# Kernel tuning notes

Measured on AMD Instinct MI355X. Metric: run time of the kernel, lower is better.

Reference implementation:

```python
import jax, jax.numpy as jnp
import numpy as np


def _conv(x, w, b=None, stride=1, pad=1, groups=1):
    y = jax.lax.conv_general_dilated(
        x, w, (stride, stride), [(pad, pad), (pad, pad)],
        dimension_numbers=('NCHW', 'OIHW', 'NCHW'), feature_group_count=groups)
    return y if b is None else y + b[None, :, None, None]


def _dwt(x):
    # Haar DWT as grouped stride-2 conv, filters pre-flipped as in the torch code
    ll = np.array([[0.5, 0.5], [0.5, 0.5]])
    lh = np.array([[-0.5, -0.5], [0.5, 0.5]])
    hl = np.array([[-0.5, 0.5], [-0.5, 0.5]])
    hh = np.array([[0.5, -0.5], [-0.5, 0.5]])
    filts = np.stack([f[None, ::-1, ::-1] for f in (ll, lh, hl, hh)], 0)  # [4,1,2,2]
    w = jnp.asarray(np.concatenate([filts] * 3, 0), x.dtype)  # [12,1,2,2], groups=3
    return _conv(x, w, None, stride=2, pad=0, groups=3)


def setup_inputs():
    key = jax.random.key(0)
    ks = iter(jax.random.split(key, 64))
    def w(*shape):
        return jax.random.normal(next(ks), shape, jnp.float32) * 0.05
    B, H, W = 4, 512, 512
    F = 32  # number_f
    d = {'x': jax.random.uniform(next(ks), (B, 3, H, W), jnp.float32)}
    d['enc1_w'] = w(F, 3, 3, 3); d['enc1_b'] = w(F)
    for i in range(2, 6):
        d['enc%d_w' % i] = w(F, F, 3, 3); d['enc%d_b' % i] = w(F)
    d['cdc_w'] = w(F, F, 3, 3)                      # central-difference conv, no bias
    d['ct_w'] = w(64, 9, 3, 3); d['ct_b'] = w(64)   # conv_theta on 9-ch high_freq
    d['t1_w'] = w(64, 64, 1, 1); d['t1_b'] = w(64)
    d['t2_w'] = w(64, 64, 1, 1); d['t2_b'] = w(64)
    d['t3_w'] = w(1, 64, 1, 1); d['t3_b'] = w(1)
    d['lf_w'] = w(64, 3, 3, 3); d['lf_b'] = w(64)   # low_freq conv on haar_A
    d['fc1_w'] = w(512, 64); d['fc1_b'] = w(512)
    d['fc2_w'] = w(512, 512); d['fc2_b'] = w(512)
    d['fc3_w'] = w(512, 512); d['fc3_b'] = w(512)
    d['g_w'] = w(F, 512); d['g_b'] = w(F)           # to_gamma_0
    d['be_w'] = w(F, 512); d['be_b'] = w(F)         # to_beta_0
    d['res_w'] = w(F, F, 3, 3); d['res_b'] = w(F)
    d['d1_w'] = w(F, F, 3, 3); d['d1_b'] = w(F)
    d['d2_w'] = w(1, F, 3, 3); d['d2_b'] = w(1)
    return d


def reference(x, enc1_w, enc1_b, enc2_w, enc2_b, enc3_w, enc3_b, enc4_w, enc4_b,
              enc5_w, enc5_b, cdc_w, ct_w, ct_b, t1_w, t1_b, t2_w, t2_b, t3_w, t3_b,
              lf_w, lf_b, fc1_w, fc1_b, fc2_w, fc2_b, fc3_w, fc3_b,
              g_w, g_b, be_w, be_b, res_w, res_b, d1_w, d1_b, d2_w, d2_b):
    relu = jax.nn.relu
    # encoder
    f = relu(_conv(x, enc1_w, enc1_b))
    f = relu(_conv(f, enc2_w, enc2_b))
    f = relu(_conv(f, enc3_w, enc3_b))
    f = relu(_conv(f, enc4_w, enc4_b))
    f_org4 = relu(_conv(f, enc5_w, enc5_b))  # [B,32,H,W]
    # Haar wavelet split: per input channel blocks of 4 = (A,H,V,D)
    dwt = _dwt(x)                             # [B,12,H/2,W/2]
    haar_A = dwt[:, 0::4]                     # c1,c5,c9
    high_freq = jnp.concatenate([dwt[:, 1::4], dwt[:, 2::4], dwt[:, 3::4]], 1)  # [B,9,...]
    # theta net (Conv2d_cd)
    a = relu(_conv(high_freq, ct_w, ct_b))
    a = a.mean((2, 3), keepdims=True)         # adaptive avg pool to 1x1
    a = relu(_conv(a, t1_w, t1_b, pad=0))
    a = relu(_conv(a, t2_w, t2_b, pad=0))
    theta = jax.nn.sigmoid(_conv(a, t3_w, t3_b, pad=0))   # [B,1,1,1]
    out_normal = _conv(f_org4, cdc_w, None)
    kdiff = cdc_w.sum((2, 3))[:, :, None, None]            # [32,32,1,1]
    out_diff = _conv(f_org4, kdiff, None, pad=0)
    f_deco = relu(out_normal - theta * out_diff)           # [B,32,H,W]
    # attention / FiLM branch
    am = relu(_conv(haar_A, lf_w, lf_b)).mean((2, 3))      # [B,64]
    am = relu(am @ fc1_w.T + fc1_b)
    am = relu(am @ fc2_w.T + fc2_b)
    am = jax.nn.sigmoid(am @ fc3_w.T + fc3_b)              # [B,512]
    gamma = jax.nn.sigmoid(am @ g_w.T + g_b)[:, :, None, None]  # [B,32,1,1]
    beta = jnp.tanh(am @ be_w.T + be_b)[:, :, None, None]
    f = f_deco + gamma * _conv(f_deco, res_w, res_b) + beta
    # decoder
    f = relu(_conv(f, d1_w, d1_b))
    out_map = jnp.tanh(_conv(f, d2_w, d2_b))               # [B,1,H,W]
    enhance_image = x + out_map * (x * x - x)
    return enhance_image, out_map
```

## Files before the change

kernel.cpp:

```cpp
#include <hip/hip_runtime.h>
#include <hip/hip_bf16.h>
#include <cmath>

#define TPB 256

typedef __attribute__((ext_vector_type(8))) short s16x8;
typedef __attribute__((ext_vector_type(4))) float f32x4;
typedef unsigned short ushortT;

constexpr long long PSTR = 8454272;
constexpr int HW = 512 * 512;

static __device__ __forceinline__ short f2bf(float f) {
    union { __hip_bfloat16 h; short s; } u;
    u.h = __float2bfloat16(f);
    return u.s;
}
static __device__ __forceinline__ float bf2f(unsigned short u) {
    union { unsigned int i; float f; } v;
    v.i = ((unsigned int)u) << 16;
    return v.f;
}
static __device__ __forceinline__ unsigned int pack2(float a, float b) {
    return (unsigned int)(unsigned short)f2bf(a) | ((unsigned int)(unsigned short)f2bf(b) << 16);
}

#define GLOAD_LDS16(gp, lp) \
    __builtin_amdgcn_global_load_lds((const __attribute__((address_space(1))) void*)(gp), \
                                     (__attribute__((address_space(3))) void*)(lp), 16, 0, 0)

static __device__ void pack_body(const float* w, const float* bias, const float* theta,
                                 short* dst, int CO, int CI_src, int ci_off, int cog, int l)
{
    const int l15 = l & 15, sl = l >> 4;
    for (int t = 0; t < 9; ++t) {
        for (int mt = 0; mt < 2; ++mt) {
            const int co = cog * 32 + 16 * mt + l15;
            s16x8 p;
            #pragma unroll
            for (int i = 0; i < 8; ++i) {
                const int pci = 8 * sl + i;
                float val = 0.f;
                if (co < CO && pci >= ci_off && pci < ci_off + CI_src) {
                    const int ci = pci - ci_off;
                    val = w[((size_t)co * CI_src + ci) * 9 + t];
                    if (theta && t == 4) {
                        float s = 0.f;
                        for (int tt = 0; tt < 9; ++tt) s += w[((size_t)co * CI_src + ci) * 9 + tt];
                        val -= theta[0] * s;
                    }
                }
                p[i] = f2bf(val);
            }
            *(s16x8*)(dst + ((size_t)(t * 2 + mt) * 64 + l) * 8) = p;
        }
    }
    if (l < 32) {
        const int co = cog * 32 + l;
        ((float*)(dst + 9216))[l] = (bias && co < CO) ? bias[co] : 0.f;
    }
}

__global__ __launch_bounds__(64) void packall_k(
    const float* e1w, const float* e1b, const float* e2w, const float* e2b,
    const float* e3w, const float* e3b, const float* e4w, const float* e4b,
    const float* e5w, const float* e5b, const float* resw, const float* resb,
    const float* d1w, const float* d1b, const float* d2w, const float* d2b,
    const float* ctw, const float* ctb, const float* lfw, const float* lfb,
    short* wpack)
{
    const int s = blockIdx.x;
    const float *w, *b;
    int CO = 32, CI = 32, coff = 0, cog = 0;
    switch (s) {
        case 0: w = e1w; b = e1b; CI = 3; break;
        case 1: w = e2w; b = e2b; break;
        case 2: w = e3w; b = e3b; break;
        case 3: w = e4w; b = e4b; break;
        case 4: w = e5w; b = e5b; break;
        case 5: w = resw; b = resb; break;
        case 6: w = d1w; b = d1b; break;
        case 7: w = d2w; b = d2b; CO = 1; break;
        case 8: case 9: w = ctw; b = ctb; CO = 64; CI = 9; cog = s - 8; break;
        default: w = lfw; b = lfb; CO = 64; CI = 3; coff = 9; cog = s - 10; break;
    }
    pack_body(w, b, nullptr, wpack + (size_t)s * 10240, CO, CI, coff, cog, threadIdx.x);
}

__global__ __launch_bounds__(64) void packcdc_k(
    const float* cdcw, const float* theta, short* wpack)
{
    const int b = blockIdx.x;
    pack_body(cdcw, nullptr, theta + b, wpack + (size_t)(12 + b) * 10240, 32, 32, 0, 0, threadIdx.x);
}

__global__ __launch_bounds__(TPB) void zero_k(unsigned int* A2u, unsigned int* B2u)
{
    const int idx = blockIdx.x * TPB + threadIdx.x;
    if (idx >= 8 * 32832) return;
    const int q = idx / 32832, r = idx % 32832;
    unsigned int* P = (q < 4 ? A2u : B2u) + (size_t)(q & 3) * 4227136;
    const int RSU = 514 * 16;
    int off;
    if (r < 8224)       off = r;
    else if (r < 16448) off = 513 * RSU + (r - 8224);
    else if (r < 24640) { int u = r - 16448; off = (1 + (u >> 4)) * RSU + (u & 15); }
    else                { int u = r - 24640; off = (1 + (u >> 4)) * RSU + 513 * 16 + (u & 15); }
    P[off] = 0u;
}

__global__ __launch_bounds__(TPB) void ctlf_k(
    const float* __restrict__ x0p, const short* __restrict__ wpack8,
    float* __restrict__ part)
{
    constexpr int RSX = 66;
    constexpr int ROWB = RSX * 64;
    __shared__ s16x8 lds_t[6 * RSX * 4];
    __shared__ float s_red[4][32];
    char* sb = (char*)lds_t;

    const int z = blockIdx.z, cog = blockIdx.y;
    const int bid = blockIdx.x;
    const int x0 = (bid & 3) * 64, y0 = (bid >> 2) * 4;
    const int tid = threadIdx.x, lane = tid & 63, wv = tid >> 6;
    const int l15 = lane & 15, slot = lane >> 4;

    const short* wslot = wpack8 + (size_t)cog * 10240;
    const float* xz = x0p + (size_t)z * 3 * HW;

    s16x8 wf[9][2];
    #pragma unroll
    for (int t = 0; t < 9; ++t)
        #pragma unroll
        for (int mt = 0; mt < 2; ++mt)
            wf[t][mt] = *(const s16x8*)(wslot + ((size_t)(t * 2 + mt) * 64 + lane) * 8);

    #pragma unroll
    for (int j = 0; j < 2; ++j) {
        const int p = j * 256 + tid;
        if (p < 396) {
            const int row = p / 66, lx = p - row * 66;
            const int vs = (lx + (lx >> 2)) & 3;
            char* base = sb + (row * RSX + lx) * 64;
            const int sy = y0 + row - 1, sx = x0 + lx - 1;
            s16x8 pk0, pk1, zz;
            #pragma unroll
            for (int i = 0; i < 8; ++i) { pk0[i] = 0; pk1[i] = 0; zz[i] = 0; }
            if (sy >= 0 && sy < 256 && sx >= 0 && sx < 256) {
                #pragma unroll
                for (int c = 0; c < 3; ++c) {
                    const float* xp = xz + ((size_t)c * 512 + 2 * sy) * 512 + 2 * sx;
                    const float2 tp = *(const float2*)xp;
                    const float2 bt = *(const float2*)(xp + 512);
                    const float a = tp.x, b = tp.y, cc = bt.x, d = bt.y;
                    pk0[c]     = f2bf(0.5f * (a + b - cc - d));
                    pk0[3 + c] = f2bf(0.5f * (a - b + cc - d));
                    const float hh = 0.5f * (a - b - cc + d);
                    const float ll = 0.5f * (a + b + cc + d);
                    if (c < 2) pk0[6 + c] = f2bf(hh);
                    else       pk1[0]     = f2bf(hh);
                    pk1[1 + c] = f2bf(ll);
                }
            }
            *(s16x8*)(base + ((0 ^ vs) << 4)) = pk0;
            *(s16x8*)(base + ((1 ^ vs) << 4)) = pk1;
            *(s16x8*)(base + ((2 ^ vs) << 4)) = zz;
            *(s16x8*)(base + ((3 ^ vs) << 4)) = zz;
        }
    }
    __syncthreads();

    const int xw = 16 * wv;
    int roff[3];
    #pragma unroll
    for (int dx = 0; dx < 3; ++dx) {
        const int lx = xw + dx + l15;
        const int vs = (lx + (lx >> 2)) & 3;
        roff[dx] = lx * 64 + ((slot ^ vs) << 4);
    }
    const float* bptr = (const float*)(wslot + 9216);

    float ps[2][4];
    #pragma unroll
    for (int mt = 0; mt < 2; ++mt)
        #pragma unroll
        for (int reg = 0; reg < 4; ++reg) ps[mt][reg] = 0.f;

    #pragma unroll
    for (int r2 = 0; r2 < 4; r2 += 2) {
        f32x4 acc[2][2];
        #pragma unroll
        for (int a = 0; a < 2; ++a)
            #pragma unroll
            for (int b = 0; b < 2; ++b)
                #pragma unroll
                for (int e = 0; e < 4; ++e) acc[a][b][e] = 0.f;

        #pragma unroll
        for (int dy = 0; dy < 3; ++dy) {
            const int rb0 = (r2 + dy) * ROWB;
            #pragma unroll
            for (int dx = 0; dx < 3; ++dx) {
                const int tap = dy * 3 + dx;
                const s16x8 b0 = *(const s16x8*)(sb + rb0 + roff[dx]);
                const s16x8 b1 = *(const s16x8*)(sb + rb0 + ROWB + roff[dx]);
                #pragma unroll
                for (int mt = 0; mt < 2; ++mt) {
                    acc[0][mt] = __builtin_amdgcn_mfma_f32_16x16x32_bf16(wf[tap][mt], b0, acc[0][mt], 0, 0, 0);
                    acc[1][mt] = __builtin_amdgcn_mfma_f32_16x16x32_bf16(wf[tap][mt], b1, acc[1][mt], 0, 0, 0);
                }
            }
        }

        #pragma unroll
        for (int rr = 0; rr < 2; ++rr)
            #pragma unroll
            for (int mt = 0; mt < 2; ++mt)
                #pragma unroll
                for (int reg = 0; reg < 4; ++reg)
                    ps[mt][reg] += fmaxf(acc[rr][mt][reg] + bptr[16 * mt + 4 * slot + reg], 0.f);
    }

    #pragma unroll
    for (int mt = 0; mt < 2; ++mt)
        #pragma unroll
        for (int reg = 0; reg < 4; ++reg) {
            #pragma unroll
            for (int o = 1; o < 16; o <<= 1)
                ps[mt][reg] += __shfl_xor(ps[mt][reg], o, 64);
        }
    #pragma unroll
    for (int mt = 0; mt < 2; ++mt)
        #pragma unroll
        for (int reg = 0; reg < 4; ++reg)
            if (l15 == mt * 4 + reg)
                s_red[wv][16 * mt + 4 * slot + reg] = ps[mt][reg];
    __syncthreads();
    if (tid < 32) {
        const float s = s_red[0][tid] + s_red[1][tid] + s_red[2][tid] + s_red[3][tid];
        part[(((size_t)z * 4 + cog) * 256 + bid) * 32 + tid] = s;
    }
}

__global__ __launch_bounds__(TPB) void enc1n_k(
    const float* __restrict__ x0p, const short* __restrict__ wslot,
    ushortT* __restrict__ outP0)
{
    constexpr int RSX = 66;
    constexpr int ROWB = RSX * 64;
    __shared__ s16x8 lds_t[6 * RSX * 4];
    char* sb = (char*)lds_t;

    const int z = blockIdx.z;
    const float* xin = x0p + (size_t)z * 3 * HW;

    const int tid = threadIdx.x, lane = tid & 63, wv = tid >> 6;
    const int bid = blockIdx.x;
    const int swz = (bid & 7) * 128 + (bid >> 3);
    const int x0 = (swz & 7) * 64, y0 = (swz >> 3) * 4;
    const int l15 = lane & 15, slot = lane >> 4;

    s16x8 wf[9][2];
    #pragma unroll
    for (int t = 0; t < 9; ++t)
        #pragma unroll
        for (int mt = 0; mt < 2; ++mt)
            wf[t][mt] = *(const s16x8*)(wslot + ((size_t)(t * 2 + mt) * 64 + lane) * 8);

    #pragma unroll
    for (int j = 0; j < 2; ++j) {
        const int p = j * 256 + tid;
        if (p < 396) {
            const int row = p / 66, lx = p - row * 66;
            const int vs = (lx + (lx >> 2)) & 3;
            char* base = sb + (row * RSX + lx) * 64;
            const int gy = y0 + row - 1, gx = x0 + lx - 1;
            s16x8 pk, zz;
            #pragma unroll
            for (int i = 0; i < 8; ++i) { pk[i] = 0; zz[i] = 0; }
            if (gy >= 0 && gy < 512 && gx >= 0 && gx < 512) {
                #pragma unroll
                for (int c = 0; c < 3; ++c)
                    pk[c] = f2bf(xin[((size_t)c * 512 + gy) * 512 + gx]);
            }
            *(s16x8*)(base + ((0 ^ vs) << 4)) = pk;
            *(s16x8*)(base + ((1 ^ vs) << 4)) = zz;
            *(s16x8*)(base + ((2 ^ vs) << 4)) = zz;
            *(s16x8*)(base + ((3 ^ vs) << 4)) = zz;
        }
    }
    __syncthreads();

    const int xw = 16 * wv;
    int roff[3];
    #pragma unroll
    for (int dx = 0; dx < 3; ++dx) {
        const int lx = xw + dx + l15;
        const int vs = (lx + (lx >> 2)) & 3;
        roff[dx] = lx * 64 + ((slot ^ vs) << 4);
    }
    const float* bptr = (const float*)(wslot + 9216);
    ushortT* outP = outP0 + (size_t)z * PSTR;

    #pragma unroll
    for (int r2 = 0; r2 < 4; r2 += 2) {
        f32x4 acc[2][2];
        #pragma unroll
        for (int a = 0; a < 2; ++a)
            #pragma unroll
            for (int b = 0; b < 2; ++b)
                #pragma unroll
                for (int e = 0; e < 4; ++e) acc[a][b][e] = 0.f;

        #pragma unroll
        for (int dy = 0; dy < 3; ++dy) {
            const int rb0 = (r2 + dy) * ROWB;
            #pragma unroll
            for (int dx = 0; dx < 3; ++dx) {
                const int tap = dy * 3 + dx;
                const s16x8 b0 = *(const s16x8*)(sb + rb0 + roff[dx]);
                const s16x8 b1 = *(const s16x8*)(sb + rb0 + ROWB + roff[dx]);
                #pragma unroll
                for (int mt = 0; mt < 2; ++mt) {
                    acc[0][mt] = __builtin_amdgcn_mfma_f32_16x16x32_bf16(wf[tap][mt], b0, acc[0][mt], 0, 0, 0);
                    acc[1][mt] = __builtin_amdgcn_mfma_f32_16x16x32_bf16(wf[tap][mt], b1, acc[1][mt], 0, 0, 0);
                }
            }
        }

        #pragma unroll
        for (int rr = 0; rr < 2; ++rr) {
            const int gy = y0 + r2 + rr;
            const int gx = x0 + xw + l15;
            #pragma unroll
            for (int mt = 0; mt < 2; ++mt) {
                const size_t off = ((size_t)(gy + 1) * 514 + gx + 1) * 32 + 16 * mt + 4 * slot;
                float v[4];
                #pragma unroll
                for (int reg = 0; reg < 4; ++reg)
                    v[reg] = fmaxf(acc[rr][mt][reg] + bptr[16 * mt + 4 * slot + reg], 0.f);
                *(uint2*)(outP + off) = make_uint2(pack2(v[0], v[1]), pack2(v[2], v[3]));
            }
        }
    }
}

template<int EPI>
__global__ __launch_bounds__(TPB) void dconv64p_k(
    const ushortT* __restrict__ inP0, const short* __restrict__ wbase, int wstr,
    ushortT* __restrict__ outP0,
    const float* __restrict__ gamma0, const float* __restrict__ beta0,
    const float* __restrict__ xorig0, float* __restrict__ outE0, float* __restrict__ outM0)
{
    constexpr int MT = (EPI == 3) ? 1 : 2;
    constexpr int RSX = 66;
    constexpr int ROWB = RSX * 64;
    constexpr int BUFB = 6 * RSX * 64;
    __shared__ s16x8 lds_t[2 * 6 * RSX * 4];
    char* sbase = (char*)lds_t;

    const int z = blockIdx.z;
    const ushortT* inP = inP0 + (size_t)z * PSTR;
    const short* wslot = wbase + (size_t)z * wstr;

    const int tid = threadIdx.x, lane = tid & 63, wv = tid >> 6;
    const int bid = blockIdx.x;
    const int xcd = bid & 7, idx = bid >> 3;
    const int x0 = (idx & 7) * 64;
    const int yband = xcd * 4 + (idx >> 3);
    const int l15 = lane & 15, slot = lane >> 4;

    s16x8 wf[9][MT];
    #pragma unroll
    for (int t = 0; t < 9; ++t)
        #pragma unroll
        for (int mt = 0; mt < MT; ++mt)
            wf[t][mt] = *(const s16x8*)(wslot + ((size_t)(t * 2 + mt) * 64 + lane) * 8);

    const int xw = 16 * wv;
    int roff[3];
    #pragma unroll
    for (int dx = 0; dx < 3; ++dx) {
        const int lx = xw + dx + l15;
        const int vs = (lx + (lx >> 2)) & 3;
        roff[dx] = lx * 64 + ((slot ^ vs) << 4);
    }
    const float* bptr = (const float*)(wslot + 9216);

    auto stage = [&](int t, int b) {
        const int y0 = yband * 16 + 4 * t;
        char* sb = sbase + b * BUFB;
        #pragma unroll
        for (int j = 0; j < 6; ++j) {
            const int p = j * 256 + tid;
            const int row = p / 264;
            const int rem = p - row * 264;
            const int lx = rem >> 2, osl = rem & 3;
            const int o = osl ^ ((lx + (lx >> 2)) & 3);
            const ushortT* gp = inP + ((size_t)(y0 + row) * 514 + x0 + lx) * 32 + o * 8;
            GLOAD_LDS16(gp, sb + (size_t)(j * 256 + wv * 64) * 16);
        }
        if (tid < 48) {
            const int p = 1536 + tid;
            const int row = p / 264;
            const int rem = p - row * 264;
            const int lx = rem >> 2, osl = rem & 3;
            const int o = osl ^ ((lx + (lx >> 2)) & 3);
            const ushortT* gp = inP + ((size_t)(y0 + row) * 514 + x0 + lx) * 32 + o * 8;
            GLOAD_LDS16(gp, sb + (size_t)1536 * 16);
        }
    };

    stage(0, 0);

    #pragma unroll 1
    for (int t = 0; t < 4; ++t) {
        __syncthreads();
        if (t < 3) stage(t + 1, (t + 1) & 1);
        char* sb = sbase + (t & 1) * BUFB;
        const int y0t = yband * 16 + 4 * t;

        #pragma unroll
        for (int r2 = 0; r2 < 4; r2 += 2) {
            f32x4 acc[2][MT];
            #pragma unroll
            for (int a = 0; a < 2; ++a)
                #pragma unroll
                for (int b = 0; b < MT; ++b)
                    #pragma unroll
                    for (int e = 0; e < 4; ++e) acc[a][b][e] = 0.f;

            #pragma unroll
            for (int dy = 0; dy < 3; ++dy) {
                const int rb0 = (r2 + dy) * ROWB;
                #pragma unroll
                for (int dx = 0; dx < 3; ++dx) {
                    const int tap = dy * 3 + dx;
                    const s16x8 b0 = *(const s16x8*)(sb + rb0 + roff[dx]);
                    const s16x8 b1 = *(const s16x8*)(sb + rb0 + ROWB + roff[dx]);
                    #pragma unroll
                    for (int mt = 0; mt < MT; ++mt) {
                        acc[0][mt] = __builtin_amdgcn_mfma_f32_16x16x32_bf16(wf[tap][mt], b0, acc[0][mt], 0, 0, 0);
                        acc[1][mt] = __builtin_amdgcn_mfma_f32_16x16x32_bf16(wf[tap][mt], b1, acc[1][mt], 0, 0, 0);
                    }
                }
            }

            #pragma unroll
            for (int rr = 0; rr < 2; ++rr) {
                const int gy = y0t + r2 + rr;
                const int gx = x0 + xw + l15;
                if constexpr (EPI == 3) {
                    if (slot == 0) {
                        const float* xorig = xorig0 + (size_t)z * 3 * HW;
                        float* outE = outE0 + (size_t)z * 3 * HW;
                        float* outM = outM0 + (size_t)z * HW;
                        const float om = tanhf(acc[rr][0][0] + bptr[0]);
                        outM[(size_t)gy * 512 + gx] = om;
                        #pragma unroll
                        for (int c = 0; c < 3; ++c) {
                            const size_t xi = ((size_t)c * 512 + gy) * 512 + gx;
                            const float xv = xorig[xi];
                            outE[xi] = xv + om * (xv * xv - xv);
                        }
                    }
                } else {
                    ushortT* outP = outP0 + (size_t)z * PSTR;
                    #pragma unroll
                    for (int mt = 0; mt < MT; ++mt) {
                        const size_t off = ((size_t)(gy + 1) * 514 + gx + 1) * 32 + 16 * mt + 4 * slot;
                        float v[4];
                        #pragma unroll
                        for (int reg = 0; reg < 4; ++reg)
                            v[reg] = acc[rr][mt][reg] + bptr[16 * mt + 4 * slot + reg];
                        if constexpr (EPI == 0) {
                            #pragma unroll
                            for (int reg = 0; reg < 4; ++reg) v[reg] = fmaxf(v[reg], 0.f);
                        } else if constexpr (EPI == 2) {
                            const int prow = r2 + rr + 1;
                            const int lxr = xw + l15 + 1;
                            const int vsr = (lxr + (lxr >> 2)) & 3;
                            const int oo = (2 * mt + (slot >> 1)) ^ vsr;
                            const uint2 din = *(const uint2*)(sb + (prow * RSX + lxr) * 64 + (oo << 4) + ((slot & 1) << 3));
                            const float* gamma = gamma0 + 32 * z;
                            const float* beta  = beta0 + 32 * z;
                            const int cb = 16 * mt + 4 * slot;
                            v[0] = bf2f((unsigned short)(din.x & 0xffff)) + gamma[cb + 0] * v[0] + beta[cb + 0];
                            v[1] = bf2f((unsigned short)(din.x >> 16))    + gamma[cb + 1] * v[1] + beta[cb + 1];
                            v[2] = bf2f((unsigned short)(din.y & 0xffff)) + gamma[cb + 2] * v[2] + beta[cb + 2];
                            v[3] = bf2f((unsigned short)(din.y >> 16))    + gamma[cb + 3] * v[3] + beta[cb + 3];
                        }
                        *(uint2*)(outP + off) = make_uint2(pack2(v[0], v[1]), pack2(v[2], v[3]));
                    }
                }
            }
        }
    }
}

__global__ __launch_bounds__(TPB) void meanfin_k(
    const float* __restrict__ part, float* __restrict__ amean, float* __restrict__ am0)
{
    const int br = blockIdx.x;
    const int o = threadIdx.x;
    const int z = o >> 6, co = o & 63;
    const int cog = (br ? 2 : 0) + (co >> 5), c = co & 31;
    const float* p = part + (((size_t)z * 4 + cog) * 256) * 32 + c;
    float s = 0.f;
    for (int j = 0; j < 256; ++j) s += p[j * 32];
    (br ? am0 : amean)[z * 64 + co] = s * (1.f / 65536.f);
}

__global__ __launch_bounds__(64) void tchain_k(
    const float* __restrict__ amean,
    const float* __restrict__ t1w, const float* __restrict__ t1b,
    const float* __restrict__ t2w, const float* __restrict__ t2b,
    const float* __restrict__ t3w, const float* __restrict__ t3b,
    float* __restrict__ theta)
{
    const int b = blockIdx.x;
    const float* am = amean + b * 64;
    __shared__ float a0[64], a1[64], a2[64];
    const int co = threadIdx.x;
    a0[co] = am[co];
    __syncthreads();
    float s = t1b[co];
    #pragma unroll 8
    for (int ci = 0; ci < 64; ++ci) s = fmaf(t1w[co * 64 + ci], a0[ci], s);
    a1[co] = fmaxf(s, 0.f);
    __syncthreads();
    s = t2b[co];
    #pragma unroll 8
    for (int ci = 0; ci < 64; ++ci) s = fmaf(t2w[co * 64 + ci], a1[ci], s);
    a2[co] = fmaxf(s, 0.f);
    __syncthreads();
    if (co == 0) {
        float v = t3b[0];
        for (int ci = 0; ci < 64; ++ci) v = fmaf(t3w[ci], a2[ci], v);
        theta[b] = 1.f / (1.f + expf(-v));
    }
}

template<int ACT>
__global__ __launch_bounds__(TPB) void fcw_k(
    const float* __restrict__ in, const float* __restrict__ w,
    const float* __restrict__ bias, float* __restrict__ out, int K, int N)
{
    const int lane = threadIdx.x & 63, wv = threadIdx.x >> 6;
    const int idx = blockIdx.x * 4 + wv;
    if (idx >= 4 * N) return;
    const int b = idx / N, co = idx % N;
    float s = 0.f;
    for (int k = lane * 4; k < K; k += 256) {
        const float4 wv4 = *(const float4*)(w + (size_t)co * K + k);
        const float4 iv  = *(const float4*)(in + (size_t)b * K + k);
        s += wv4.x * iv.x + wv4.y * iv.y + wv4.z * iv.z + wv4.w * iv.w;
    }
    #pragma unroll
    for (int o = 32; o > 0; o >>= 1) s += __shfl_xor(s, o, 64);
    if (lane == 0) {
        s += bias[co];
        if (ACT == 0) s = fmaxf(s, 0.f);
        else if (ACT == 1) s = 1.f / (1.f + expf(-s));
        else s = tanhf(s);
        out[(size_t)b * N + co] = s;
    }
}

extern "C" void kernel_launch(void* const* d_in, const int* in_sizes, int n_in,
                              void* d_out, int out_size, void* d_ws, size_t ws_size,
                              hipStream_t stream)
{
    const float* x      = (const float*)d_in[0];
    const float* cdc_w  = (const float*)d_in[11];
    const float* t1_w   = (const float*)d_in[14];
    const float* t1_b   = (const float*)d_in[15];
    const float* t2_w   = (const float*)d_in[16];
    const float* t2_b   = (const float*)d_in[17];
    const float* t3_w   = (const float*)d_in[18];
    const float* t3_b   = (const float*)d_in[19];
    const float* fc1_w  = (const float*)d_in[22];
    const float* fc1_b  = (const float*)d_in[23];
    const float* fc2_w  = (const float*)d_in[24];
    const float* fc2_b  = (const float*)d_in[25];
    const float* fc3_w  = (const float*)d_in[26];
    const float* fc3_b  = (const float*)d_in[27];
    const float* g_w    = (const float*)d_in[28];
    const float* g_b    = (const float*)d_in[29];
    const float* be_w   = (const float*)d_in[30];
    const float* be_b   = (const float*)d_in[31];

    float* out = (float*)d_out;

    ushortT* A2 = (ushortT*)d_ws;
    ushortT* B2 = A2 + 4 * PSTR;
    float* part  = (float*)(B2 + 4 * PSTR);
    float* amean = part + 131072;
    float* am0   = amean + 256;
    float* am1   = am0 + 256;
    float* am2   = am1 + 2048;
    float* am3   = am2 + 2048;
    float* theta = am3 + 2048;
    float* gamma = theta + 4;
    float* beta  = gamma + 128;
    short* wpack = (short*)(beta + 128);
    const size_t need_bytes = (size_t)((char*)(wpack + 16 * 10240) - (char*)d_ws);
    if (ws_size < need_bytes) return;

    const dim3 blk(TPB);

    packall_k<<<dim3(12), dim3(64), 0, stream>>>(
        (const float*)d_in[1], (const float*)d_in[2], (const float*)d_in[3], (const float*)d_in[4],
        (const float*)d_in[5], (const float*)d_in[6], (const float*)d_in[7], (const float*)d_in[8],
        (const float*)d_in[9], (const float*)d_in[10], (const float*)d_in[32], (const float*)d_in[33],
        (const float*)d_in[34], (const float*)d_in[35], (const float*)d_in[36], (const float*)d_in[37],
        (const float*)d_in[12], (const float*)d_in[13], (const float*)d_in[20], (const float*)d_in[21],
        wpack);

    zero_k<<<dim3((8 * 32832 + TPB - 1) / TPB), blk, 0, stream>>>((unsigned int*)A2, (unsigned int*)B2);

    ctlf_k<<<dim3(256, 4, 4), blk, 0, stream>>>(x, wpack + 8 * 10240, part);

    meanfin_k<<<dim3(2), blk, 0, stream>>>(part, amean, am0);
    tchain_k<<<dim3(4), dim3(64), 0, stream>>>(amean, t1_w, t1_b, t2_w, t2_b, t3_w, t3_b, theta);
    fcw_k<0><<<dim3(512), blk, 0, stream>>>(am0, fc1_w, fc1_b, am1, 64, 512);
    fcw_k<0><<<dim3(512), blk, 0, stream>>>(am1, fc2_w, fc2_b, am2, 512, 512);
    fcw_k<1><<<dim3(512), blk, 0, stream>>>(am2, fc3_w, fc3_b, am3, 512, 512);
    fcw_k<1><<<dim3(32), blk, 0, stream>>>(am3, g_w, g_b, gamma, 512, 32);
    fcw_k<2><<<dim3(32), blk, 0, stream>>>(am3, be_w, be_b, beta, 512, 32);
    packcdc_k<<<dim3(4), dim3(64), 0, stream>>>(cdc_w, theta, wpack);

    const dim3 gE(1024, 1, 4);
    const dim3 gP(256, 1, 4);
    float* outM = out + (size_t)4 * 3 * HW;

    enc1n_k<<<gE, blk, 0, stream>>>(x, wpack, A2);
    dconv64p_k<0><<<gP, blk, 0, stream>>>(A2, wpack + 1 * 10240, 0, B2, nullptr, nullptr, nullptr, nullptr, nullptr);
    dconv64p_k<0><<<gP, blk, 0, stream>>>(B2, wpack + 2 * 10240, 0, A2, nullptr, nullptr, nullptr, nullptr, nullptr);
    dconv64p_k<0><<<gP, blk, 0, stream>>>(A2, wpack + 3 * 10240, 0, B2, nullptr, nullptr, nullptr, nullptr, nullptr);
    dconv64p_k<0><<<gP, blk, 0, stream>>>(B2, wpack + 4 * 10240, 0, A2, nullptr, nullptr, nullptr, nullptr, nullptr);
    dconv64p_k<0><<<gP, blk, 0, stream>>>(A2, wpack + 12 * 10240, 10240, B2, nullptr, nullptr, nullptr, nullptr, nullptr);
    dconv64p_k<2><<<gP, blk, 0, stream>>>(B2, wpack + 5 * 10240, 0, A2, gamma, beta, nullptr, nullptr, nullptr);
    dconv64p_k<0><<<gP, blk, 0, stream>>>(A2, wpack + 6 * 10240, 0, B2, nullptr, nullptr, nullptr, nullptr, nullptr);
    dconv64p_k<3><<<gP, blk, 0, stream>>>(B2, wpack + 7 * 10240, 0, nullptr, nullptr, nullptr, x, out, outM);
}
```

Before: 332.5 us.

## Fuse pairs of consecutive 3x3 convs into one kernel with LDS intermediate halo tile

Replaces eight separate 32-channel conv launches with four launches, each computing two chained 3x3 convs per 64x4 output tile. The first conv's output, including a one-pixel halo, is kept in shared memory, so the intermediate activation is never written to or re-read from global memory. The cost is redundant halo recomputation (an 8x70 input tile for 4x64 outputs) and the loss of the old double-buffered multi-row pipelining. Each block is also smaller, and the grid grows to 1024 blocks per image.

```diff
diff --git a/kernel.cpp b/kernel.cpp
--- a/kernel.cpp
+++ b/kernel.cpp
@@ -346,36 +346,117 @@
 }
 
 template<int EPI>
-__global__ __launch_bounds__(TPB) void dconv64p_k(
-    const ushortT* __restrict__ inP0, const short* __restrict__ wbase, int wstr,
+__global__ __launch_bounds__(TPB) void fconv2_k(
+    const ushortT* __restrict__ inP0,
+    const short* __restrict__ w1base, int w1str,
+    const short* __restrict__ w2base,
     ushortT* __restrict__ outP0,
     const float* __restrict__ gamma0, const float* __restrict__ beta0,
     const float* __restrict__ xorig0, float* __restrict__ outE0, float* __restrict__ outM0)
 {
-    constexpr int MT = (EPI == 3) ? 1 : 2;
-    constexpr int RSX = 66;
-    constexpr int ROWB = RSX * 64;
-    constexpr int BUFB = 6 * RSX * 64;
-    __shared__ s16x8 lds_t[2 * 6 * RSX * 4];
-    char* sbase = (char*)lds_t;
+    constexpr int MT2 = (EPI == 3) ? 1 : 2;
+    constexpr int RSIN = 70;
+    constexpr int RSI  = 68;
+    constexpr int INROW = RSIN * 64;
+    constexpr int IROW  = RSI * 64;
+    __shared__ s16x8 lds_t[(8 * RSIN + 6 * RSI) * 4];
+    char* sbIN = (char*)lds_t;
+    char* sbI  = sbIN + 8 * INROW;
 
     const int z = blockIdx.z;
     const ushortT* inP = inP0 + (size_t)z * PSTR;
-    const short* wslot = wbase + (size_t)z * wstr;
+    const short* w1 = w1base + (size_t)z * w1str;
 
     const int tid = threadIdx.x, lane = tid & 63, wv = tid >> 6;
     const int bid = blockIdx.x;
-    const int xcd = bid & 7, idx = bid >> 3;
-    const int x0 = (idx & 7) * 64;
-    const int yband = xcd * 4 + (idx >> 3);
+    const int swz = (bid & 7) * 128 + (bid >> 3);
+    const int x0 = (swz & 7) * 64, y0 = (swz >> 3) * 4;
     const int l15 = lane & 15, slot = lane >> 4;
 
-    s16x8 wf[9][MT];
+    #pragma unroll
+    for (int j = 0; j < 9; ++j) {
+        const int p = j * 256 + tid;
+        if (p < 2240) {
+            const int row = p / 280;
+            const int rem = p - row * 280;
+            const int ix = rem >> 2, osl = rem & 3;
+            const int o = osl ^ ((ix + (ix >> 2)) & 3);
+            int prow = y0 - 1 + row; prow = prow < 0 ? 0 : (prow > 513 ? 513 : prow);
+            int pcol = x0 - 2 + ix;  pcol = pcol < 0 ? 0 : (pcol > 513 ? 513 : pcol);
+            const ushortT* gp = inP + ((size_t)prow * 514 + pcol) * 32 + o * 8;
+            GLOAD_LDS16(gp, sbIN + (size_t)p * 16);
+        }
+    }
+
+    s16x8 wf[9][2];
     #pragma unroll
     for (int t = 0; t < 9; ++t)
         #pragma unroll
-        for (int mt = 0; mt < MT; ++mt)
-            wf[t][mt] = *(const s16x8*)(wslot + ((size_t)(t * 2 + mt) * 64 + lane) * 8);
+        for (int mt = 0; mt < 2; ++mt)
+            wf[t][mt] = *(const s16x8*)(w1 + ((size_t)(t * 2 + mt) * 64 + lane) * 8);
+    const float* b1ptr = (const float*)(w1 + 9216);
+
+    __syncthreads();
+
+    #pragma unroll 1
+    for (int u = wv; u < 15; u += 4) {
+        const int nt1 = u % 5, rp = u / 5;
+        f32x4 a1[2][2];
+        #pragma unroll
+        for (int a = 0; a < 2; ++a)
+            #pragma unroll
+            for (int b = 0; b < 2; ++b)
+                #pragma unroll
+                for (int e = 0; e < 4; ++e) a1[a][b][e] = 0.f;
+
+        #pragma unroll
+        for (int dy = 0; dy < 3; ++dy) {
+            #pragma unroll
+            for (int dx = 0; dx < 3; ++dx) {
+                int ix = 16 * nt1 + l15 + 1 + dx; if (ix > 69) ix = 69;
+                const int co = (slot ^ ((ix + (ix >> 2)) & 3)) << 4;
+                const char* pb = sbIN + ix * 64 + co;
+                const s16x8 b0 = *(const s16x8*)(pb + (2 * rp + dy) * INROW);
+                const s16x8 b1 = *(const s16x8*)(pb + (2 * rp + dy + 1) * INROW);
+                const int tap = dy * 3 + dx;
+                #pragma unroll
+                for (int mt = 0; mt < 2; ++mt) {
+                    a1[0][mt] = __builtin_amdgcn_mfma_f32_16x16x32_bf16(wf[tap][mt], b0, a1[0][mt], 0, 0, 0);
+                    a1[1][mt] = __builtin_amdgcn_mfma_f32_16x16x32_bf16(wf[tap][mt], b1, a1[1][mt], 0, 0, 0);
+                }
+            }
+        }
+
+        const int ggx = x0 - 1 + 16 * nt1 + l15;
+        int ii = 16 * nt1 + l15; if (ii > 66) ii = 66;
+        const int vsw = (ii + (ii >> 2)) & 3;
+        #pragma unroll
+        for (int rr = 0; rr < 2; ++rr) {
+            const int gy1 = y0 - 1 + 2 * rp + rr;
+            const bool valid = ((unsigned)ggx < 512u) && ((unsigned)gy1 < 512u);
+            #pragma unroll
+            for (int mt = 0; mt < 2; ++mt) {
+                float v[4];
+                #pragma unroll
+                for (int reg = 0; reg < 4; ++reg) {
+                    v[reg] = fmaxf(a1[rr][mt][reg] + b1ptr[16 * mt + 4 * slot + reg], 0.f);
+                    if (!valid) v[reg] = 0.f;
+                }
+                const int oct = (2 * mt + (slot >> 1)) ^ vsw;
+                *(uint2*)(sbI + ((2 * rp + rr) * RSI + ii) * 64 + (oct << 4) + ((slot & 1) << 3)) =
+                    make_uint2(pack2(v[0], v[1]), pack2(v[2], v[3]));
+            }
+        }
+    }
+
+    __syncthreads();
+
+    #pragma unroll
+    for (int t = 0; t < 9; ++t)
+        #pragma unroll
+        for (int mt = 0; mt < MT2; ++mt)
+            wf[t][mt] = *(const s16x8*)(w2base + ((size_t)(t * 2 + mt) * 64 + lane) * 8);
+    const float* b2ptr = (const float*)(w2base + 9216);
 
     const int xw = 16 * wv;
     int roff[3];
@@ -385,113 +466,77 @@
         const int vs = (lx + (lx >> 2)) & 3;
         roff[dx] = lx * 64 + ((slot ^ vs) << 4);
     }
-    const float* bptr = (const float*)(wslot + 9216);
-
-    auto stage = [&](int t, int b) {
-        const int y0 = yband * 16 + 4 * t;
-        char* sb = sbase + b * BUFB;
-        #pragma unroll
-        for (int j = 0; j < 6; ++j) {
-            const int p = j * 256 + tid;
-            const int row = p / 264;
-            const int rem = p - row * 264;
-            const int lx = rem >> 2, osl = rem & 3;
-            const int o = osl ^ ((lx + (lx >> 2)) & 3);
-            const ushortT* gp = inP + ((size_t)(y0 + row) * 514 + x0 + lx) * 32 + o * 8;
-            GLOAD_LDS16(gp, sb + (size_t)(j * 256 + wv * 64) * 16);
-        }
-        if (tid < 48) {
-            const int p = 1536 + tid;
-            const int row = p / 264;
-            const int rem = p - row * 264;
-            const int lx = rem >> 2, osl = rem & 3;
-            const int o = osl ^ ((lx + (lx >> 2)) & 3);
-            const ushortT* gp = inP + ((size_t)(y0 + row) * 514 + x0 + lx) * 32 + o * 8;
-            GLOAD_LDS16(gp, sb + (size_t)1536 * 16);
-        }
-    };
-
-    stage(0, 0);
-
-    #pragma unroll 1
-    for (int t = 0; t < 4; ++t) {
-        __syncthreads();
-        if (t < 3) stage(t + 1, (t + 1) & 1);
-        char* sb = sbase + (t & 1) * BUFB;
-        const int y0t = yband * 16 + 4 * t;
-
-        #pragma unroll
-        for (int r2 = 0; r2 < 4; r2 += 2) {
-            f32x4 acc[2][MT];
-            #pragma unroll
-            for (int a = 0; a < 2; ++a)
-                #pragma unroll
-                for (int b = 0; b < MT; ++b)
+
+    #pragma unroll
+    for (int r2 = 0; r2 < 4; r2 += 2) {
+        f32x4 acc[2][MT2];
+        #pragma unroll
+        for (int a = 0; a < 2; ++a)
+            #pragma unroll
+            for (int b = 0; b < MT2; ++b)
+                #pragma unroll
+                for (int e = 0; e < 4; ++e) acc[a][b][e] = 0.f;
+
+        #pragma unroll
+        for (int dy = 0; dy < 3; ++dy) {
+            const int rb0 = (r2 + dy) * IROW;
+            #pragma unroll
+            for (int dx = 0; dx < 3; ++dx) {
+                const int tap = dy * 3 + dx;
+                const s16x8 b0 = *(const s16x8*)(sbI + rb0 + roff[dx]);
+                const s16x8 b1 = *(const s16x8*)(sbI + rb0 + IROW + roff[dx]);
+                #pragma unroll
+                for (int mt = 0; mt < MT2; ++mt) {
+                    acc[0][mt] = __builtin_amdgcn_mfma_f32_16x16x32_bf16(wf[tap][mt], b0, acc[0][mt], 0, 0, 0);
+                    acc[1][mt] = __builtin_amdgcn_mfma_f32_16x16x32_bf16(wf[tap][mt], b1, acc[1][mt], 0, 0, 0);
+                }
+            }
+        }
+
+        #pragma unroll
+        for (int rr = 0; rr < 2; ++rr) {
+            const int gy = y0 + r2 + rr;
+            const int gx = x0 + xw + l15;
+            if constexpr (EPI == 3) {
+                if (slot == 0) {
+                    const float* xorig = xorig0 + (size_t)z * 3 * HW;
+                    float* outE = outE0 + (size_t)z * 3 * HW;
+                    float* outM = outM0 + (size_t)z * HW;
+                    const float om = tanhf(acc[rr][0][0] + b2ptr[0]);
+                    outM[(size_t)gy * 512 + gx] = om;
                     #pragma unroll
-                    for (int e = 0; e < 4; ++e) acc[a][b][e] = 0.f;
-
-            #pragma unroll
-            for (int dy = 0; dy < 3; ++dy) {
-                const int rb0 = (r2 + dy) * ROWB;
-                #pragma unroll
-                for (int dx = 0; dx < 3; ++dx) {
-                    const int tap = dy * 3 + dx;
-                    const s16x8 b0 = *(const s16x8*)(sb + rb0 + roff[dx]);
-                    const s16x8 b1 = *(const s16x8*)(sb + rb0 + ROWB + roff[dx]);
+                    for (int c = 0; c < 3; ++c) {
+                        const size_t xi = ((size_t)c * 512 + gy) * 512 + gx;
+                        const float xv = xorig[xi];
+                        outE[xi] = xv + om * (xv * xv - xv);
+                    }
+                }
+            } else {
+                ushortT* outP = outP0 + (size_t)z * PSTR;
+                #pragma unroll
+                for (int mt = 0; mt < MT2; ++mt) {
+                    const size_t off = ((size_t)(gy + 1) * 514 + gx + 1) * 32 + 16 * mt + 4 * slot;
+                    float v[4];
                     #pragma unroll
-                    for (int mt = 0; mt < MT; ++mt) {
-                        acc[0][mt] = __builtin_amdgcn_mfma_f32_16x16x32_bf16(wf[tap][mt], b0, acc[0][mt], 0, 0, 0);
-                        acc[1][mt] = __builtin_amdgcn_mfma_f32_16x16x32_bf16(wf[tap][mt], b1, acc[1][mt], 0, 0, 0);
+                    for (int reg = 0; reg < 4; ++reg)
+                        v[reg] = acc[rr][mt][reg] + b2ptr[16 * mt + 4 * slot + reg];
+                    if constexpr (EPI == 0) {
+                        #pragma unroll
+                        for (int reg = 0; reg < 4; ++reg) v[reg] = fmaxf(v[reg], 0.f);
+                    } else if constexpr (EPI == 2) {
+                        const int iir = xw + l15 + 1;
+                        const int vsr = (iir + (iir >> 2)) & 3;
+                        const int oo = (2 * mt + (slot >> 1)) ^ vsr;
+                        const uint2 din = *(const uint2*)(sbI + ((r2 + rr + 1) * RSI + iir) * 64 + (oo << 4) + ((slot & 1) << 3));
+                        const float* gamma = gamma0 + 32 * z;
+                        const float* beta  = beta0 + 32 * z;
+                        const int cb = 16 * mt + 4 * slot;
+                        v[0] = bf2f((unsigned short)(din.x & 0xffff)) + gamma[cb + 0] * v[0] + beta[cb + 0];
+                        v[1] = bf2f((unsigned short)(din.x >> 16))    + gamma[cb + 1] * v[1] + beta[cb + 1];
+                        v[2] = bf2f((unsigned short)(din.y & 0xffff)) + gamma[cb + 2] * v[2] + beta[cb + 2];
+                        v[3] = bf2f((unsigned short)(din.y >> 16))    + gamma[cb + 3] * v[3] + beta[cb + 3];
                     }
-                }
-            }
-
-            #pragma unroll
-            for (int rr = 0; rr < 2; ++rr) {
-                const int gy = y0t + r2 + rr;
-                const int gx = x0 + xw + l15;
-                if constexpr (EPI == 3) {
-                    if (slot == 0) {
-                        const float* xorig = xorig0 + (size_t)z * 3 * HW;
-                        float* outE = outE0 + (size_t)z * 3 * HW;
-                        float* outM = outM0 + (size_t)z * HW;
-                        const float om = tanhf(acc[rr][0][0] + bptr[0]);
-                        outM[(size_t)gy * 512 + gx] = om;
-                        #pragma unroll
-                        for (int c = 0; c < 3; ++c) {
-                            const size_t xi = ((size_t)c * 512 + gy) * 512 + gx;
-                            const float xv = xorig[xi];
-                            outE[xi] = xv + om * (xv * xv - xv);
-                        }
-                    }
-                } else {
-                    ushortT* outP = outP0 + (size_t)z * PSTR;
-                    #pragma unroll
-                    for (int mt = 0; mt < MT; ++mt) {
-                        const size_t off = ((size_t)(gy + 1) * 514 + gx + 1) * 32 + 16 * mt + 4 * slot;
-                        float v[4];
-                        #pragma unroll
-                        for (int reg = 0; reg < 4; ++reg)
-                            v[reg] = acc[rr][mt][reg] + bptr[16 * mt + 4 * slot + reg];
-                        if constexpr (EPI == 0) {
-                            #pragma unroll
-                            for (int reg = 0; reg < 4; ++reg) v[reg] = fmaxf(v[reg], 0.f);
-                        } else if constexpr (EPI == 2) {
-                            const int prow = r2 + rr + 1;
-                            const int lxr = xw + l15 + 1;
-                            const int vsr = (lxr + (lxr >> 2)) & 3;
-                            const int oo = (2 * mt + (slot >> 1)) ^ vsr;
-                            const uint2 din = *(const uint2*)(sb + (prow * RSX + lxr) * 64 + (oo << 4) + ((slot & 1) << 3));
-                            const float* gamma = gamma0 + 32 * z;
-                            const float* beta  = beta0 + 32 * z;
-                            const int cb = 16 * mt + 4 * slot;
-                            v[0] = bf2f((unsigned short)(din.x & 0xffff)) + gamma[cb + 0] * v[0] + beta[cb + 0];
-                            v[1] = bf2f((unsigned short)(din.x >> 16))    + gamma[cb + 1] * v[1] + beta[cb + 1];
-                            v[2] = bf2f((unsigned short)(din.y & 0xffff)) + gamma[cb + 2] * v[2] + beta[cb + 2];
-                            v[3] = bf2f((unsigned short)(din.y >> 16))    + gamma[cb + 3] * v[3] + beta[cb + 3];
-                        }
-                        *(uint2*)(outP + off) = make_uint2(pack2(v[0], v[1]), pack2(v[2], v[3]));
-                    }
+                    *(uint2*)(outP + off) = make_uint2(pack2(v[0], v[1]), pack2(v[2], v[3]));
                 }
             }
         }
@@ -630,17 +675,16 @@
     fcw_k<2><<<dim3(32), blk, 0, stream>>>(am3, be_w, be_b, beta, 512, 32);
     packcdc_k<<<dim3(4), dim3(64), 0, stream>>>(cdc_w, theta, wpack);
 
-    const dim3 gE(1024, 1, 4);
-    const dim3 gP(256, 1, 4);
+    const dim3 gN(1024, 1, 4);
     float* outM = out + (size_t)4 * 3 * HW;
 
-    enc1n_k<<<gE, blk, 0, stream>>>(x, wpack, A2);
-    dconv64p_k<0><<<gP, blk, 0, stream>>>(A2, wpack + 1 * 10240, 0, B2, nullptr, nullptr, nullptr, nullptr, nullptr);
-    dconv64p_k<0><<<gP, blk, 0, stream>>>(B2, wpack + 2 * 10240, 0, A2, nullptr, nullptr, nullptr, nullptr, nullptr);
-    dconv64p_k<0><<<gP, blk, 0, stream>>>(A2, wpack + 3 * 10240, 0, B2, nullptr, nullptr, nullptr, nullptr, nullptr);
-    dconv64p_k<0><<<gP, blk, 0, stream>>>(B2, wpack + 4 * 10240, 0, A2, nullptr, nullptr, nullptr, nullptr, nullptr);
-    dconv64p_k<0><<<gP, blk, 0, stream>>>(A2, wpack + 12 * 10240, 10240, B2, nullptr, nullptr, nullptr, nullptr, nullptr);
-    dconv64p_k<2><<<gP, blk, 0, stream>>>(B2, wpack + 5 * 10240, 0, A2, gamma, beta, nullptr, nullptr, nullptr);
-    dconv64p_k<0><<<gP, blk, 0, stream>>>(A2, wpack + 6 * 10240, 0, B2, nullptr, nullptr, nullptr, nullptr, nullptr);
-    dconv64p_k<3><<<gP, blk, 0, stream>>>(B2, wpack + 7 * 10240, 0, nullptr, nullptr, nullptr, x, out, outM);
-}
+    enc1n_k<<<gN, blk, 0, stream>>>(x, wpack, A2);
+    fconv2_k<0><<<gN, blk, 0, stream>>>(A2, wpack + 1 * 10240, 0, wpack + 2 * 10240, B2,
+        nullptr, nullptr, nullptr, nullptr, nullptr);
+    fconv2_k<0><<<gN, blk, 0, stream>>>(B2, wpack + 3 * 10240, 0, wpack + 4 * 10240, A2,
+        nullptr, nullptr, nullptr, nullptr, nullptr);
+    fconv2_k<2><<<gN, blk, 0, stream>>>(A2, wpack + 12 * 10240, 10240, wpack + 5 * 10240, B2,
+        gamma, beta, nullptr, nullptr, nullptr);
+    fconv2_k<3><<<gN, blk, 0, stream>>>(B2, wpack + 6 * 10240, 0, wpack + 7 * 10240, nullptr,
+        nullptr, nullptr, x, out, outM);
+}
```

New measurement: 382.9 us. 1.15x slower.
